# Optimization experiments

Hardware: AMD Instinct MI355X
Metric: run time of the kernel (lower is better)

Reference implementation:

```python
import jax, jax.numpy as jnp
import numpy as np
from jax import lax

TAU = 2.0  # SynapseFilter time constant (learnable=False)


def setup_inputs() -> dict:
    key = jax.random.key(0)
    T, N, C, D_out = 64, 16, 128, 256
    k1, k2 = jax.random.split(key)
    x = jax.random.uniform(k1, (T, N, C, 2), dtype=jnp.float32)  # spike-like input (T,N,C,2)
    # matches torch init: _log_delay = log(linspace(1e-7, 1, D_out)).view(-1,1)
    log_delay = jnp.log(jnp.linspace(1e-7, 1.0, D_out, dtype=jnp.float32)).reshape(D_out, 1)
    log_weight = jnp.log(jnp.float32(2.0))
    # uniform noise replacing torch.bernoulli(p) (u < p  <=>  bernoulli(p))
    noise = jax.random.uniform(k2, (N, C, D_out, 2), dtype=jnp.float32)
    return {"x": x, "log_delay": log_delay, "log_weight": log_weight, "noise": noise}


def reference(x, log_delay, log_weight, noise):
    T, N, C, _ = x.shape
    D_out = log_delay.shape[0]

    # delay property: cat([exp(log_delay), flip(exp(log_delay))], dim=1) -> (D_out, 2)
    d = jnp.exp(log_delay)                      # (D_out, 1)
    delay = jnp.concatenate([d, d[::-1]], axis=1)  # (D_out, 2)

    # stochastic rounding of T * delay, broadcast to (N, C, D_out, 2)
    scaled = jnp.broadcast_to((T * delay)[None, None], (N, C, D_out, 2))
    fl = jnp.floor(scaled)
    rounded = fl + (noise < (scaled - fl)).astype(scaled.dtype)

    # clamp(max = T - 1 - argmax over time). argmax of the repeated tensor equals
    # argmax of x broadcast over D_out, so compute it cheaply on x.
    am = jnp.argmax(x, axis=0)                  # (N, C, 2)
    max_d = (T - 1 - am)[:, :, None, :]         # (N, C, 1, 2)
    rd = jnp.minimum(rounded.astype(jnp.int32), max_d.astype(jnp.int32))  # (N,C,D_out,2)

    # circular delay-line shift: out[t] = in[(t - delay) mod T]
    out_rep = jnp.broadcast_to(x[:, :, :, None, :], (T, N, C, D_out, 2))
    t_idx = jnp.arange(T, dtype=jnp.int32)[:, None, None, None, None]
    idx = (t_idx - rd[None]) % T                # (T, N, C, D_out, 2)
    shifted = jnp.take_along_axis(out_rep, idx, axis=0)

    # SynapseFilter (multi-step): y_t = y_{t-1} * (1 - 1/tau) + x_t, y_{-1}=0
    decay = jnp.float32(1.0 - 1.0 / TAU)

    def step(carry, xt):
        carry = carry * decay + xt
        return carry, carry

    _, y = lax.scan(step, jnp.zeros_like(shifted[0]), shifted)  # (T,N,C,D_out,2)

    # scale by weight = exp(log_weight), sum over D_in=2
    out = (y * jnp.exp(log_weight)).sum(axis=-1)  # (T, N, C, D_out)
    return out
```

## Files before the change

kernel.cpp:

```cpp
#include <hip/hip_runtime.h>
#include <math.h>

#define T_STEPS 64
#define D_OUT 256

__global__ __launch_bounds__(256) void jeffress_kernel(
    const float* __restrict__ x,
    const float* __restrict__ log_delay,
    const float* __restrict__ log_weight,
    const float* __restrict__ noise,
    float* __restrict__ out,
    int NC)
{
    __shared__ float xs0[T_STEPS];
    __shared__ float xs1[T_STEPS];
    __shared__ int maxd[2];

    const int nc = blockIdx.x;
    const int j  = threadIdx.x;

    if (j < T_STEPS) {
        const float* xp = x + ((size_t)j * NC + nc) * 2;
        xs0[j] = xp[0];
        xs1[j] = xp[1];
    }
    __syncthreads();

    if (j < 2) {
        const float* xsrc = (j == 0) ? xs0 : xs1;
        float best = xsrc[0];
        int bi = 0;
        for (int t = 1; t < T_STEPS; ++t) {
            float v = xsrc[t];
            if (v > best) { best = v; bi = t; }
        }
        maxd[j] = (T_STEPS - 1) - bi;
    }
    __syncthreads();

    double ld0 = (double)log_delay[j];
    double ld1 = (double)log_delay[(D_OUT - 1) - j];
    double s0 = (double)T_STEPS * exp(ld0);
    double s1 = (double)T_STEPS * exp(ld1);
    double f0 = floor(s0), f1 = floor(s1);

    const float* nptr = noise + ((size_t)nc * D_OUT + j) * 2;
    float n0 = nptr[0], n1 = nptr[1];

    int r0 = (int)f0 + (((double)n0 < (s0 - f0)) ? 1 : 0);
    int r1 = (int)f1 + (((double)n1 < (s1 - f1)) ? 1 : 0);
    int rd0 = min(r0, maxd[0]);
    int rd1 = min(r1, maxd[1]);

    const float w = (float)exp((double)log_weight[0]);

    float y0 = 0.f, y1 = 0.f;
    float* op = out + (size_t)nc * D_OUT + j;
    const size_t ostride = (size_t)NC * D_OUT;
    #pragma unroll
    for (int t = 0; t < T_STEPS; ++t) {
        y0 = y0 * 0.5f + xs0[(t - rd0) & (T_STEPS - 1)];
        y1 = y1 * 0.5f + xs1[(t - rd1) & (T_STEPS - 1)];
        op[(size_t)t * ostride] = (y0 + y1) * w;
    }
}

extern "C" void kernel_launch(void* const* d_in, const int* in_sizes, int n_in,
                              void* d_out, int out_size, void* d_ws, size_t ws_size,
                              hipStream_t stream) {
    const float* x          = (const float*)d_in[0];
    const float* log_delay  = (const float*)d_in[1];
    const float* log_weight = (const float*)d_in[2];
    const float* noise      = (const float*)d_in[3];
    float* out = (float*)d_out;

    const int NC = in_sizes[3] / (D_OUT * 2);

    jeffress_kernel<<<NC, D_OUT, 0, stream>>>(x, log_delay, log_weight, noise, out, NC);
}
```

Before: 145.4 us.

## Process four NC rows per block with four outputs per thread and vector stores

Each block now handles four (n,c) rows, and each thread computes four consecutive D_out outputs. Its noise loads become float4 and its output writes become 128-bit nontemporal stores. The double-precision exp/floor of the delay table is computed once per block into shared memory and reused across the four rows, which cuts per-thread FP64 work. The cost is fewer blocks, more registers per thread, and an assumption that NC is divisible by 4.

```diff
diff --git a/kernel.cpp b/kernel.cpp
--- a/kernel.cpp
+++ b/kernel.cpp
@@ -3,6 +3,9 @@
 
 #define T_STEPS 64
 #define D_OUT 256
+#define NCB 4
+
+typedef float vfloat4 __attribute__((ext_vector_type(4)));
 
 __global__ __launch_bounds__(256) void jeffress_kernel(
     const float* __restrict__ x,
@@ -12,56 +15,84 @@
     float* __restrict__ out,
     int NC)
 {
-    __shared__ float xs0[T_STEPS];
-    __shared__ float xs1[T_STEPS];
-    __shared__ int maxd[2];
+    __shared__ float  xs0[NCB][T_STEPS];
+    __shared__ float  xs1[NCB][T_STEPS];
+    __shared__ double fracd[D_OUT];
+    __shared__ int    flo[D_OUT];
+    __shared__ int    maxd[NCB][2];
 
-    const int nc = blockIdx.x;
-    const int j  = threadIdx.x;
+    const int tid = threadIdx.x;
+    const int nc_base = blockIdx.x * NCB;
+    const int lnc = tid >> 6;
+    const int jj  = tid & 63;
+    const int nc  = nc_base + lnc;
 
-    if (j < T_STEPS) {
-        const float* xp = x + ((size_t)j * NC + nc) * 2;
-        xs0[j] = xp[0];
-        xs1[j] = xp[1];
+    {
+        int t = tid >> 2;
+        int l = tid & 3;
+        const float* xp = x + ((size_t)t * NC + nc_base + l) * 2;
+        xs0[l][t] = xp[0];
+        xs1[l][t] = xp[1];
+    }
+    {
+        double s = (double)T_STEPS * exp((double)log_delay[tid]);
+        double f = floor(s);
+        fracd[tid] = s - f;
+        flo[tid]   = (int)f;
     }
     __syncthreads();
 
-    if (j < 2) {
-        const float* xsrc = (j == 0) ? xs0 : xs1;
-        float best = xsrc[0];
-        int bi = 0;
+    if (tid < NCB * 2) {
+        int l = tid >> 1, i = tid & 1;
+        const float* xsrc = i ? xs1[l] : xs0[l];
+        float best = xsrc[0]; int bi = 0;
         for (int t = 1; t < T_STEPS; ++t) {
             float v = xsrc[t];
             if (v > best) { best = v; bi = t; }
         }
-        maxd[j] = (T_STEPS - 1) - bi;
+        maxd[l][i] = (T_STEPS - 1) - bi;
     }
     __syncthreads();
 
-    double ld0 = (double)log_delay[j];
-    double ld1 = (double)log_delay[(D_OUT - 1) - j];
-    double s0 = (double)T_STEPS * exp(ld0);
-    double s1 = (double)T_STEPS * exp(ld1);
-    double f0 = floor(s0), f1 = floor(s1);
+    const float* nptr = noise + ((size_t)nc * D_OUT + 4 * jj) * 2;
+    float4 na = *(const float4*)(nptr);
+    float4 nb = *(const float4*)(nptr + 4);
+    float n0i[4] = { na.x, na.z, nb.x, nb.z };
+    float n1i[4] = { na.y, na.w, nb.y, nb.w };
 
-    const float* nptr = noise + ((size_t)nc * D_OUT + j) * 2;
-    float n0 = nptr[0], n1 = nptr[1];
+    const int md0 = maxd[lnc][0];
+    const int md1 = maxd[lnc][1];
 
-    int r0 = (int)f0 + (((double)n0 < (s0 - f0)) ? 1 : 0);
-    int r1 = (int)f1 + (((double)n1 < (s1 - f1)) ? 1 : 0);
-    int rd0 = min(r0, maxd[0]);
-    int rd1 = min(r1, maxd[1]);
+    int rd0[4], rd1[4];
+    #pragma unroll
+    for (int c = 0; c < 4; ++c) {
+        int j  = 4 * jj + c;
+        int jf = (D_OUT - 1) - j;
+        int r0 = flo[j]  + (((double)n0i[c] < fracd[j])  ? 1 : 0);
+        int r1 = flo[jf] + (((double)n1i[c] < fracd[jf]) ? 1 : 0);
+        rd0[c] = min(r0, md0);
+        rd1[c] = min(r1, md1);
+    }
 
     const float w = (float)exp((double)log_weight[0]);
 
-    float y0 = 0.f, y1 = 0.f;
-    float* op = out + (size_t)nc * D_OUT + j;
+    float y0[4] = {0.f, 0.f, 0.f, 0.f};
+    float y1[4] = {0.f, 0.f, 0.f, 0.f};
+    const float* xr0 = xs0[lnc];
+    const float* xr1 = xs1[lnc];
+    float* op = out + ((size_t)nc) * D_OUT + 4 * jj;
     const size_t ostride = (size_t)NC * D_OUT;
+
     #pragma unroll
     for (int t = 0; t < T_STEPS; ++t) {
-        y0 = y0 * 0.5f + xs0[(t - rd0) & (T_STEPS - 1)];
-        y1 = y1 * 0.5f + xs1[(t - rd1) & (T_STEPS - 1)];
-        op[(size_t)t * ostride] = (y0 + y1) * w;
+        vfloat4 o;
+        #pragma unroll
+        for (int c = 0; c < 4; ++c) {
+            y0[c] = y0[c] * 0.5f + xr0[(t - rd0[c]) & (T_STEPS - 1)];
+            y1[c] = y1[c] * 0.5f + xr1[(t - rd1[c]) & (T_STEPS - 1)];
+            o[c] = (y0[c] + y1[c]) * w;
+        }
+        __builtin_nontemporal_store(o, (vfloat4*)(op + (size_t)t * ostride));
     }
 }
 
@@ -76,5 +107,5 @@
 
     const int NC = in_sizes[3] / (D_OUT * 2);
 
-    jeffress_kernel<<<NC, D_OUT, 0, stream>>>(x, log_delay, log_weight, noise, out, NC);
+    jeffress_kernel<<<NC / NCB, 256, 0, stream>>>(x, log_delay, log_weight, noise, out, NC);
 }
```

New measurement: 148.9 us. 1.02x slower.
